# Kernel optimization log

Measured on AMD Instinct MI355X. Metric: run time of the kernel, lower is better.

## Reference

```python
import jax, jax.numpy as jnp
import numpy as np

N = 20000
E = 200000
F_IN = 23
H1, C1 = 8, 120   # gat1: heads=8, out=120 -> concat dim 960
D1 = H1 * C1
H2, C2 = 1, 1     # gat2: heads=1, out=1
NEG_SLOPE = 0.2


def _gatv2_layer(x, src, dst, Wl, bl, Wr, br, att, bias, H, C):
    """GATv2Conv (PyG semantics, share_weights=False, concat).
    x: [N, F]; src/dst: [E] (messages flow src -> dst).
    """
    n = x.shape[0]
    xl = (x @ Wl + bl).reshape(n, H, C)   # source-side transform
    xr = (x @ Wr + br).reshape(n, H, C)   # target-side transform
    # per-edge attention logit: a^T LeakyReLU(xl[j] + xr[i])
    s = jax.nn.leaky_relu(xl[src] + xr[dst], NEG_SLOPE)   # [E, H, C]
    e = jnp.einsum('ehc,hc->eh', s, att)                  # [E, H]
    # segment softmax over incoming edges of each target node
    m = jax.ops.segment_max(e, dst, num_segments=n)       # [N, H]
    ex = jnp.exp(e - m[dst])
    denom = jax.ops.segment_sum(ex, dst, num_segments=n)  # [N, H]
    alpha = ex / (denom[dst] + 1e-16)                     # [E, H]
    out = jax.ops.segment_sum(alpha[:, :, None] * xl[src], dst, num_segments=n)
    return out.reshape(n, H * C) + bias


def setup_inputs() -> dict:
    key = jax.random.key(0)
    ks = jax.random.split(key, 14)
    x = jax.random.normal(ks[0], (N, F_IN), dtype=jnp.float32)
    edge_index = jax.random.randint(ks[1], (2, E), 0, N, dtype=jnp.int64)
    def lin(k, fin, fout):
        return jax.random.normal(k, (fin, fout), dtype=jnp.float32) / np.float32(np.sqrt(fin))
    return {
        'x': x,
        'edge_index': edge_index,
        'W1l': lin(ks[2], F_IN, D1), 'b1l': jnp.zeros((D1,), jnp.float32),
        'W1r': lin(ks[3], F_IN, D1), 'b1r': jnp.zeros((D1,), jnp.float32),
        'att1': jax.random.normal(ks[4], (H1, C1), dtype=jnp.float32) / np.float32(np.sqrt(C1)),
        'bias1': jnp.zeros((D1,), jnp.float32),
        'W2l': lin(ks[5], D1, H2 * C2), 'b2l': jnp.zeros((H2 * C2,), jnp.float32),
        'W2r': lin(ks[6], D1, H2 * C2), 'b2r': jnp.zeros((H2 * C2,), jnp.float32),
        'att2': jax.random.normal(ks[7], (H2, C2), dtype=jnp.float32),
        'bias2': jnp.zeros((H2 * C2,), jnp.float32),
    }


def reference(x, edge_index, W1l, b1l, W1r, b1r, att1, bias1,
              W2l, b2l, W2r, b2r, att2, bias2):
    # add self loops (PyG GATv2Conv default add_self_loops=True)
    loops = jnp.arange(N, dtype=edge_index.dtype)
    src = jnp.concatenate([edge_index[0], loops])
    dst = jnp.concatenate([edge_index[1], loops])
    h = _gatv2_layer(x, src, dst, W1l, b1l, W1r, b1r, att1, bias1, H1, C1)
    h = jax.nn.relu(h)
    # F.dropout treated as identity (deterministic/eval reference)
    out = _gatv2_layer(h, src, dst, W2l, b2l, W2r, b2r, att2, bias2, H2, C2)
    return out  # [N, 1]
```

## Files before the change

### kernel.cpp

```cpp
#include <hip/hip_runtime.h>
#include <hip/hip_fp16.h>
#include <math.h>

#define N    20000
#define E    200000
#define EP   220000
#define F_IN 23
#define D1   960
#define H1   8
#define C1   120
#define KPL  15
#define PC   16
#define ROW  1024

typedef _Float16 f16x2 __attribute__((ext_vector_type(2)));
typedef unsigned int u32x4 __attribute__((ext_vector_type(4)));

__device__ inline float fdot2(__half2 a, __half2 b, float c) {
#if __has_builtin(__builtin_amdgcn_fdot2)
  f16x2 av, bv;
  __builtin_memcpy(&av, &a, 4);
  __builtin_memcpy(&bv, &b, 4);
  return __builtin_amdgcn_fdot2(av, bv, c, false);
#else
  float2 af = __half22float2(a), bf = __half22float2(b);
  return fmaf(af.x, bf.x, fmaf(af.y, bf.y, c));
#endif
}

__device__ inline __half2 hmax2(__half2 a, __half2 b) {
  f16x2 av, bv;
  __builtin_memcpy(&av, &a, 4);
  __builtin_memcpy(&bv, &b, 4);
  f16x2 rv = __builtin_elementwise_max(av, bv);
  __half2 r;
  __builtin_memcpy(&r, &rv, 4);
  return r;
}

#define T1_BLOCKS 250
#define T1_NPB    80
#define T1_TILE   8
#define CNT_BLOCKS 230
__global__ __launch_bounds__(960, 4)
void k_t1_count(const float* __restrict__ x,
                const float* __restrict__ W1l, const float* __restrict__ b1l,
                const float* __restrict__ W1r, const float* __restrict__ b1r,
                __half* __restrict__ xl1, __half* __restrict__ xr1,
                const int* __restrict__ ei, int* __restrict__ deg,
                int* __restrict__ dcnt,
                int* __restrict__ off, int* __restrict__ cursor) {
  int tid = threadIdx.x;
  __shared__ union {
    struct {
      __half lbL[T1_TILE][ROW];
      __half lbR[T1_TILE][ROW];
      float  xs[T1_TILE][F_IN];
    } t;
    struct { int parts[960]; int wsum[16]; } sc;
  } sh;
  __shared__ bool slast;

  if (blockIdx.x >= T1_BLOCKS) {
    int id = (blockIdx.x - T1_BLOCKS) * 960 + tid;
    if (id < EP) {
      int dst = (id < E) ? ei[E + id] : (id - E);
      atomicAdd(&deg[dst], 1);
    }
    __syncthreads();
    if (tid == 0) {
      __threadfence();
      slast = (atomicAdd(dcnt, 1) == CNT_BLOCKS - 1);
    }
    __syncthreads();
    if (!slast) return;
    int base = tid * 21;
    int loc[21];
    int run = 0;
#pragma unroll
    for (int e = 0; e < 21; e++) {
      int i = base + e;
      int v = (i < N) ? __hip_atomic_load(&deg[i], __ATOMIC_RELAXED,
                                          __HIP_MEMORY_SCOPE_AGENT)
                      : 0;
      loc[e] = run;
      run += v;
    }
    sh.sc.parts[tid] = run;
    __syncthreads();
    int lane = tid & 63, wid = tid >> 6;
    int v = sh.sc.parts[tid];
    int incl = v;
#pragma unroll
    for (int d = 1; d < 64; d <<= 1) {
      int t = __shfl_up(incl, d, 64);
      if (lane >= d) incl += t;
    }
    if (lane == 63) sh.sc.wsum[wid] = incl;
    __syncthreads();
    if (tid == 0) {
      int acc = 0;
#pragma unroll
      for (int w = 0; w < 15; w++) { int t = sh.sc.wsum[w]; sh.sc.wsum[w] = acc; acc += t; }
      sh.sc.wsum[15] = acc;
    }
    __syncthreads();
    int texcl = incl - v + sh.sc.wsum[wid];
#pragma unroll
    for (int e = 0; e < 21; e++) {
      int i = base + e;
      if (i < N) { int t = texcl + loc[e]; off[i] = t; cursor[i] = t; }
    }
    if (tid == 0) off[N] = sh.sc.wsum[15];
    return;
  }

  int rlane = tid / 15;
  int k = tid - rlane * 15;
  int c = (rlane >> 3) * C1 + (rlane & 7) * KPL + k;
  int pidx = rlane * PC + k;
  float wl[F_IN], wr[F_IN];
#pragma unroll
  for (int f = 0; f < F_IN; f++) {
    wl[f] = W1l[f * D1 + c];
    wr[f] = W1r[f * D1 + c];
  }
  float blv = b1l[c], brv = b1r[c];

  if (tid < 64 * T1_TILE) {
    int r = tid >> 6, l = tid & 63;
    sh.t.lbL[r][l * PC + 15] = __ushort_as_half((unsigned short)0);
    sh.t.lbR[r][l * PC + 15] = __ushort_as_half((unsigned short)0);
  }

  int nbase = blockIdx.x * T1_NPB;
  for (int t = 0; t < T1_NPB; t += T1_TILE) {
    if (tid < T1_TILE * F_IN) {
      int n = tid / F_IN, f = tid - n * F_IN;
      sh.t.xs[n][f] = x[(size_t)(nbase + t + n) * F_IN + f];
    }
    __syncthreads();
#pragma unroll
    for (int n = 0; n < T1_TILE; n++) {
      float al = blv, ar = brv;
#pragma unroll
      for (int f = 0; f < F_IN; f++) {
        float xv = sh.t.xs[n][f];
        al = fmaf(xv, wl[f], al);
        ar = fmaf(xv, wr[f], ar);
      }
      sh.t.lbL[n][pidx] = __float2half(al);
      sh.t.lbR[n][pidx] = __float2half(ar);
    }
    __syncthreads();
    const u32x4* lbLu = (const u32x4*)sh.t.lbL;
    const u32x4* lbRu = (const u32x4*)sh.t.lbR;
    for (int i = tid; i < 2 * T1_TILE * 128; i += 960) {
      int arr = i >> 10;
      int j = i & 1023;
      int r = j >> 7, o = j & 127;
      u32x4 val = arr ? lbRu[j] : lbLu[j];
      u32x4* dst = (u32x4*)((arr ? xr1 : xl1) + ((size_t)(nbase + t + r) << 10)) + o;
      __builtin_nontemporal_store(val, dst);
    }
  }
}

__global__ __launch_bounds__(512)
void k_scatter(const int* __restrict__ ei, int* __restrict__ cursor,
               int* __restrict__ srcs) {
  int id = blockIdx.x * 512 + threadIdx.x;
  if (id >= EP) return;
  int dst, src;
  if (id < E) { dst = ei[E + id]; src = ei[id]; }
  else        { dst = id - E;     src = id - E; }
  int pos = atomicAdd(&cursor[dst], 1);
  srcs[pos] = src;
}

union Rowu {
  uint4 u[2];
  __half2 h[8];
};

__global__ __launch_bounds__(256)
void k_l1agg(const int* __restrict__ off, const int* __restrict__ srcs,
             const __half* __restrict__ xl1, const __half* __restrict__ xr1,
             const float* __restrict__ att1, const float* __restrict__ bias1,
             const float* __restrict__ W2l, const float* __restrict__ b2l,
             const float* __restrict__ W2r, const float* __restrict__ b2r,
             float* __restrict__ xl2, float* __restrict__ xr2) {
  int node = blockIdx.x * 4 + (threadIdx.x >> 6);
  if (node >= N) return;
  int lane = threadIdx.x & 63;
  int cbase = (lane >> 3) * C1 + (lane & 7) * KPL;

  Rowu xr;
  {
    const uint4* rp = (const uint4*)(xr1 + ((size_t)node << 10)) + (lane << 1);
    xr.u[0] = rp[0]; xr.u[1] = rp[1];
  }
  __half2 at2[8];
#pragma unroll
  for (int j = 0; j < 7; j++)
    at2[j] = __floats2half2_rn(att1[cbase + 2 * j], att1[cbase + 2 * j + 1]);
  at2[7] = __floats2half2_rn(att1[cbase + 14], 0.f);

  const __half2 c02 = __float2half2_rn(0.2f);
  __half2 o2[8];
#pragma unroll
  for (int j = 0; j < 8; j++) o2[j] = __float2half2_rn(0.f);
  float m = -INFINITY, d = 0.f;

  int p0 = off[node], p1 = off[node + 1];
  int sA = srcs[p0];
  int sB = srcs[(p0 + 1 < p1) ? p0 + 1 : p1 - 1];
  Rowu rA, rB;
  {
    const uint4* rp = (const uint4*)(xl1 + ((size_t)sA << 10)) + (lane << 1);
    rA.u[0] = rp[0]; rA.u[1] = rp[1];
    const uint4* np = (const uint4*)(xl1 + ((size_t)sB << 10)) + (lane << 1);
    rB.u[0] = np[0]; rB.u[1] = np[1];
  }

  for (int p = p0; p < p1; p++) {
    Rowu cur = rA;
    rA = rB;
    int pn = (p + 2 < p1) ? p + 2 : p1 - 1;
    int sn = srcs[pn];
    const uint4* np = (const uint4*)(xl1 + ((size_t)sn << 10)) + (lane << 1);
    rB.u[0] = np[0]; rB.u[1] = np[1];

    float pe = 0.f;
#pragma unroll
    for (int j = 0; j < 8; j++) {
      __half2 s = __hadd2(cur.h[j], xr.h[j]);
      __half2 l = hmax2(s, __hmul2(c02, s));
      pe = fdot2(l, at2[j], pe);
    }
    pe += __shfl_xor(pe, 1, 64);
    pe += __shfl_xor(pe, 2, 64);
    pe += __shfl_xor(pe, 4, 64);
    if (pe > m) {
      float sc = __expf(m - pe);
      d *= sc;
      __half2 s2 = __float2half2_rn(sc);
#pragma unroll
      for (int j = 0; j < 8; j++) o2[j] = __hmul2(o2[j], s2);
      m = pe;
    }
    float w = __expf(pe - m);
    d += w;
    __half2 w2 = __float2half2_rn(w);
#pragma unroll
    for (int j = 0; j < 8; j++) o2[j] = __hfma2(w2, cur.h[j], o2[j]);
  }

  float inv = 1.f / (d + 1e-16f);
  float pl = 0.f, pr = 0.f;
#pragma unroll
  for (int j = 0; j < 8; j++) {
    float2 of = __half22float2(o2[j]);
    int k0 = 2 * j;
    float hv = fmaf(of.x, inv, bias1[cbase + k0]);
    hv = fmaxf(hv, 0.f);
    pl = fmaf(hv, W2l[cbase + k0], pl);
    pr = fmaf(hv, W2r[cbase + k0], pr);
    if (j < 7) {
      float hv2 = fmaf(of.y, inv, bias1[cbase + k0 + 1]);
      hv2 = fmaxf(hv2, 0.f);
      pl = fmaf(hv2, W2l[cbase + k0 + 1], pl);
      pr = fmaf(hv2, W2r[cbase + k0 + 1], pr);
    }
  }
#pragma unroll
  for (int dx = 1; dx < 64; dx <<= 1) {
    pl += __shfl_xor(pl, dx, 64);
    pr += __shfl_xor(pr, dx, 64);
  }
  if (lane == 0) {
    xl2[node] = pl + b2l[0];
    xr2[node] = pr + b2r[0];
  }
}

__global__ void k_l2agg(const int* __restrict__ off, const int* __restrict__ srcs,
                        const float* __restrict__ xl2, const float* __restrict__ xr2,
                        const float* __restrict__ att2, const float* __restrict__ bias2,
                        float* __restrict__ out) {
  int node = blockIdx.x * blockDim.x + threadIdx.x;
  if (node >= N) return;
  float xr = xr2[node];
  float a2 = att2[0];
  float m = -INFINITY, d = 0.f, o = 0.f;
  int p1 = off[node + 1];
  for (int p = off[node]; p < p1; p++) {
    float xl = xl2[srcs[p]];
    float s = xl + xr;
    s = fmaxf(s, 0.2f * s);
    float e = s * a2;
    if (e > m) { float sc = __expf(m - e); d *= sc; o *= sc; m = e; }
    float w = __expf(e - m);
    d += w;
    o = fmaf(w, xl, o);
  }
  out[node] = o / (d + 1e-16f) + bias2[0];
}

extern "C" void kernel_launch(void* const* d_in, const int* in_sizes, int n_in,
                              void* d_out, int out_size, void* d_ws, size_t ws_size,
                              hipStream_t stream) {
  const float* x     = (const float*)d_in[0];
  const int*   ei    = (const int*)d_in[1];
  const float* W1l   = (const float*)d_in[2];
  const float* b1l   = (const float*)d_in[3];
  const float* W1r   = (const float*)d_in[4];
  const float* b1r   = (const float*)d_in[5];
  const float* att1  = (const float*)d_in[6];
  const float* bias1 = (const float*)d_in[7];
  const float* W2l   = (const float*)d_in[8];
  const float* b2l   = (const float*)d_in[9];
  const float* W2r   = (const float*)d_in[10];
  const float* b2r   = (const float*)d_in[11];
  const float* att2  = (const float*)d_in[12];
  const float* bias2 = (const float*)d_in[13];
  float* out = (float*)d_out;

  char* ws = (char*)d_ws;
  size_t off_b = 0;
  auto alloc = [&](size_t bytes) {
    size_t cur = off_b;
    off_b += (bytes + 255) & ~(size_t)255;
    return (void*)(ws + cur);
  };
  __half* xl1 = (__half*)alloc((size_t)N * ROW * sizeof(__half));
  __half* xr1 = (__half*)alloc((size_t)N * ROW * sizeof(__half));
  int*   deg  = (int*)alloc((size_t)(N + 1) * sizeof(int));
  int*   offp = (int*)alloc((size_t)(N + 1) * sizeof(int));
  int*   curs = (int*)alloc((size_t)N * sizeof(int));
  int*   srcs = (int*)alloc((size_t)EP * sizeof(int));
  float* xl2  = (float*)alloc((size_t)N * sizeof(float));
  float* xr2  = (float*)alloc((size_t)N * sizeof(float));
  int*   dcnt = deg + N;
  (void)ws_size; (void)in_sizes; (void)n_in; (void)out_size;

  (void)hipMemsetAsync(deg, 0, (size_t)(N + 1) * sizeof(int), stream);

  k_t1_count<<<T1_BLOCKS + CNT_BLOCKS, 960, 0, stream>>>(
      x, W1l, b1l, W1r, b1r, xl1, xr1, ei, deg, dcnt, offp, curs);

  k_scatter<<<(EP + 511) / 512, 512, 0, stream>>>(ei, curs, srcs);

  k_l1agg<<<(N + 3) / 4, 256, 0, stream>>>(
      offp, srcs, xl1, xr1, att1, bias1, W2l, b2l, W2r, b2r, xl2, xr2);

  k_l2agg<<<(N + 255) / 256, 256, 0, stream>>>(
      offp, srcs, xl2, xr2, att2, bias2, out);
}
```

Measured before the change: 177.6 us.

## Split degree counting into own kernel and use fp16 dot2 for layer-1 transform

```diff
diff --git a/kernel.cpp b/kernel.cpp
--- a/kernel.cpp
+++ b/kernel.cpp
@@ -38,51 +38,46 @@
   return r;
 }
 
+__global__ __launch_bounds__(512)
+void k_count(const int* __restrict__ ei, int* __restrict__ deg) {
+  int id = blockIdx.x * 512 + threadIdx.x;
+  if (id >= EP) return;
+  int dst = (id < E) ? ei[E + id] : (id - E);
+  atomicAdd(&deg[dst], 1);
+}
+
 #define T1_BLOCKS 250
 #define T1_NPB    80
 #define T1_TILE   8
-#define CNT_BLOCKS 230
-__global__ __launch_bounds__(960, 4)
-void k_t1_count(const float* __restrict__ x,
-                const float* __restrict__ W1l, const float* __restrict__ b1l,
-                const float* __restrict__ W1r, const float* __restrict__ b1r,
-                __half* __restrict__ xl1, __half* __restrict__ xr1,
-                const int* __restrict__ ei, int* __restrict__ deg,
-                int* __restrict__ dcnt,
-                int* __restrict__ off, int* __restrict__ cursor) {
+union WU { u32x4 q[6]; __half2 h[24]; };
+union XU { u32x4 q[3]; __half2 h[12]; };
+
+__global__ __launch_bounds__(960)
+void k_t1_scan(const float* __restrict__ x,
+               const float* __restrict__ W1l, const float* __restrict__ b1l,
+               const float* __restrict__ W1r, const float* __restrict__ b1r,
+               __half* __restrict__ xl1, __half* __restrict__ xr1,
+               const int* __restrict__ deg,
+               int* __restrict__ off, int* __restrict__ cursor) {
   int tid = threadIdx.x;
   __shared__ union {
     struct {
-      __half lbL[T1_TILE][ROW];
-      __half lbR[T1_TILE][ROW];
-      float  xs[T1_TILE][F_IN];
+      __half  wlds[960][48];
+      __half  lbL[T1_TILE][ROW];
+      __half  lbR[T1_TILE][ROW];
+      __half2 xs2[T1_TILE][12];
     } t;
     struct { int parts[960]; int wsum[16]; } sc;
   } sh;
-  __shared__ bool slast;
 
   if (blockIdx.x >= T1_BLOCKS) {
-    int id = (blockIdx.x - T1_BLOCKS) * 960 + tid;
-    if (id < EP) {
-      int dst = (id < E) ? ei[E + id] : (id - E);
-      atomicAdd(&deg[dst], 1);
-    }
-    __syncthreads();
-    if (tid == 0) {
-      __threadfence();
-      slast = (atomicAdd(dcnt, 1) == CNT_BLOCKS - 1);
-    }
-    __syncthreads();
-    if (!slast) return;
     int base = tid * 21;
     int loc[21];
     int run = 0;
 #pragma unroll
     for (int e = 0; e < 21; e++) {
       int i = base + e;
-      int v = (i < N) ? __hip_atomic_load(&deg[i], __ATOMIC_RELAXED,
-                                          __HIP_MEMORY_SCOPE_AGENT)
-                      : 0;
+      int v = (i < N) ? deg[i] : 0;
       loc[e] = run;
       run += v;
     }
@@ -119,12 +114,13 @@
   int k = tid - rlane * 15;
   int c = (rlane >> 3) * C1 + (rlane & 7) * KPL + k;
   int pidx = rlane * PC + k;
-  float wl[F_IN], wr[F_IN];
-#pragma unroll
+
   for (int f = 0; f < F_IN; f++) {
-    wl[f] = W1l[f * D1 + c];
-    wr[f] = W1r[f * D1 + c];
-  }
+    sh.t.wlds[tid][f]      = __float2half(W1l[f * D1 + c]);
+    sh.t.wlds[tid][24 + f] = __float2half(W1r[f * D1 + c]);
+  }
+  sh.t.wlds[tid][23] = __ushort_as_half((unsigned short)0);
+  sh.t.wlds[tid][47] = __ushort_as_half((unsigned short)0);
   float blv = b1l[c], brv = b1r[c];
 
   if (tid < 64 * T1_TILE) {
@@ -132,22 +128,35 @@
     sh.t.lbL[r][l * PC + 15] = __ushort_as_half((unsigned short)0);
     sh.t.lbR[r][l * PC + 15] = __ushort_as_half((unsigned short)0);
   }
+  __syncthreads();
 
   int nbase = blockIdx.x * T1_NPB;
   for (int t = 0; t < T1_NPB; t += T1_TILE) {
-    if (tid < T1_TILE * F_IN) {
-      int n = tid / F_IN, f = tid - n * F_IN;
-      sh.t.xs[n][f] = x[(size_t)(nbase + t + n) * F_IN + f];
-    }
-    __syncthreads();
+    if (tid < T1_TILE * 12) {
+      int n = tid / 12, j = tid - n * 12;
+      const float* xp = &x[(size_t)(nbase + t + n) * F_IN];
+      float f0 = xp[2 * j];
+      float f1 = (2 * j + 1 < F_IN) ? xp[2 * j + 1] : 0.f;
+      sh.t.xs2[n][j] = __floats2half2_rn(f0, f1);
+    }
+    __syncthreads();
+
+    WU w;
+    const u32x4* wp = (const u32x4*)&sh.t.wlds[tid][0];
+#pragma unroll
+    for (int q = 0; q < 6; q++) w.q[q] = wp[q];
+
 #pragma unroll
     for (int n = 0; n < T1_TILE; n++) {
+      XU xu;
+      const u32x4* xp = (const u32x4*)&sh.t.xs2[n][0];
+#pragma unroll
+      for (int q = 0; q < 3; q++) xu.q[q] = xp[q];
       float al = blv, ar = brv;
 #pragma unroll
-      for (int f = 0; f < F_IN; f++) {
-        float xv = sh.t.xs[n][f];
-        al = fmaf(xv, wl[f], al);
-        ar = fmaf(xv, wr[f], ar);
+      for (int j = 0; j < 12; j++) {
+        al = fdot2(w.h[j],      xu.h[j], al);
+        ar = fdot2(w.h[12 + j], xu.h[j], ar);
       }
       sh.t.lbL[n][pidx] = __float2half(al);
       sh.t.lbR[n][pidx] = __float2half(ar);
@@ -335,19 +344,20 @@
   };
   __half* xl1 = (__half*)alloc((size_t)N * ROW * sizeof(__half));
   __half* xr1 = (__half*)alloc((size_t)N * ROW * sizeof(__half));
-  int*   deg  = (int*)alloc((size_t)(N + 1) * sizeof(int));
+  int*   deg  = (int*)alloc((size_t)N * sizeof(int));
   int*   offp = (int*)alloc((size_t)(N + 1) * sizeof(int));
   int*   curs = (int*)alloc((size_t)N * sizeof(int));
   int*   srcs = (int*)alloc((size_t)EP * sizeof(int));
   float* xl2  = (float*)alloc((size_t)N * sizeof(float));
   float* xr2  = (float*)alloc((size_t)N * sizeof(float));
-  int*   dcnt = deg + N;
   (void)ws_size; (void)in_sizes; (void)n_in; (void)out_size;
 
-  (void)hipMemsetAsync(deg, 0, (size_t)(N + 1) * sizeof(int), stream);
-
-  k_t1_count<<<T1_BLOCKS + CNT_BLOCKS, 960, 0, stream>>>(
-      x, W1l, b1l, W1r, b1r, xl1, xr1, ei, deg, dcnt, offp, curs);
+  (void)hipMemsetAsync(deg, 0, (size_t)N * sizeof(int), stream);
+
+  k_count<<<(EP + 511) / 512, 512, 0, stream>>>(ei, deg);
+
+  k_t1_scan<<<T1_BLOCKS + 1, 960, 0, stream>>>(
+      x, W1l, b1l, W1r, b1r, xl1, xr1, deg, offp, curs);
 
   k_scatter<<<(EP + 511) / 512, 512, 0, stream>>>(ei, curs, srcs);
 
```

New measurement: 144.8 us (median of 3 runs). 1.23x faster.
